# Optimization experiments

Measured on AMD Instinct MI355X. Metric: run time of the kernel, lower is better.

## Reference

```python
import jax, jax.numpy as jnp
import numpy as np

D_MODEL = 256
N_LAYER = 8
N_HEAD = 8
D_K = D_MODEL // N_HEAD  # 32
D_FF = 4 * D_MODEL
VOCAB = 5
NUM_BUCKETS = 64
MAX_DIST = 256
L = 768
B = 1
EPS = 1e-5


def _ln(x, s, b):
    m = jnp.mean(x, axis=-1, keepdims=True)
    v = jnp.mean((x - m) ** 2, axis=-1, keepdims=True)
    return (x - m) * jax.lax.rsqrt(v + EPS) * s + b


def _rp_bucket(rel_pos):
    # faithful to RelativePositionBias._relative_position_bucket
    nb = NUM_BUCKETS // 2  # 32
    ret = (rel_pos < 0).astype(jnp.int32) * nb
    arp = jnp.abs(rel_pos)
    max_exact = nb // 2  # 16
    is_small = arp < max_exact
    safe = jnp.maximum(arp, 1).astype(jnp.float32)
    log_ratio = float(np.log(MAX_DIST / max_exact))
    vil = max_exact + (jnp.log(safe / max_exact) / log_ratio * (nb - max_exact)).astype(jnp.int32)
    vil = jnp.minimum(vil, nb - 1)
    return ret + jnp.where(is_small, arp.astype(jnp.int32), vil)


def setup_inputs() -> dict:
    key = jax.random.key(0)
    ks = iter(jax.random.split(key, 40))
    s = 0.02
    d = {}
    d['seq'] = jax.random.randint(next(ks), (B, L), 0, VOCAB, dtype=jnp.int32)
    d['tok_emb'] = jax.random.normal(next(ks), (VOCAB, D_MODEL), jnp.float32) * s
    d['rp_emb'] = jax.random.normal(next(ks), (NUM_BUCKETS, N_HEAD), jnp.float32) * s
    # stacked per-layer params [N_LAYER, ...]
    d['wq'] = jax.random.normal(next(ks), (N_LAYER, D_MODEL, D_MODEL), jnp.float32) * s
    d['wk'] = jax.random.normal(next(ks), (N_LAYER, D_MODEL, D_MODEL), jnp.float32) * s
    d['wv'] = jax.random.normal(next(ks), (N_LAYER, D_MODEL, D_MODEL), jnp.float32) * s
    d['wo'] = jax.random.normal(next(ks), (N_LAYER, D_MODEL, D_MODEL), jnp.float32) * s
    d['ln1_s'] = jnp.ones((N_LAYER, D_MODEL), jnp.float32)
    d['ln1_b'] = jnp.zeros((N_LAYER, D_MODEL), jnp.float32)
    d['ln2_s'] = jnp.ones((N_LAYER, D_MODEL), jnp.float32)
    d['ln2_b'] = jnp.zeros((N_LAYER, D_MODEL), jnp.float32)
    d['ffn_w1'] = jax.random.normal(next(ks), (N_LAYER, D_MODEL, D_FF), jnp.float32) * s
    d['ffn_b1'] = jnp.zeros((N_LAYER, D_FF), jnp.float32)
    d['ffn_w2'] = jax.random.normal(next(ks), (N_LAYER, D_FF, D_MODEL), jnp.float32) * s
    d['ffn_b2'] = jnp.zeros((N_LAYER, D_MODEL), jnp.float32)
    d['lnf_s'] = jnp.ones((D_MODEL,), jnp.float32)
    d['lnf_b'] = jnp.zeros((D_MODEL,), jnp.float32)
    d['pair_q_w'] = jax.random.normal(next(ks), (D_MODEL, D_MODEL), jnp.float32) * s
    d['pair_q_b'] = jnp.zeros((D_MODEL,), jnp.float32)
    d['pair_k_w'] = jax.random.normal(next(ks), (D_MODEL, D_MODEL), jnp.float32) * s
    d['pair_k_b'] = jnp.zeros((D_MODEL,), jnp.float32)
    d['pair_rp_emb'] = jax.random.normal(next(ks), (NUM_BUCKETS, D_MODEL), jnp.float32) * s
    d['cls_w1'] = jax.random.normal(next(ks), (D_MODEL, D_MODEL), jnp.float32) * s
    d['cls_b1'] = jnp.zeros((D_MODEL,), jnp.float32)
    d['cls_w2'] = jax.random.normal(next(ks), (D_MODEL, 2), jnp.float32) * s
    d['cls_b2'] = jnp.zeros((2,), jnp.float32)
    return d


def reference(seq, tok_emb, rp_emb, wq, wk, wv, wo, ln1_s, ln1_b, ln2_s, ln2_b,
              ffn_w1, ffn_b1, ffn_w2, ffn_b2, lnf_s, lnf_b,
              pair_q_w, pair_q_b, pair_k_w, pair_k_b, pair_rp_emb,
              cls_w1, cls_b1, cls_w2, cls_b2):
    scale = D_K ** 0.5
    x = tok_emb[seq]  # [B, L, D]
    pos = jnp.arange(L)
    rel = pos[:, None] - pos[None, :]  # [L, L]
    bucket = _rp_bucket(rel)  # [L, L] int32
    bias = jnp.transpose(rp_emb[bucket], (2, 0, 1))[None]  # [1, H, L, L]

    def step(x, p):
        Wq, Wk, Wv, Wo, s1, b1, s2, b2, fw1, fb1, fw2, fb2 = p
        h = _ln(x, s1, b1)
        q = (h @ Wq).reshape(B, L, N_HEAD, D_K).transpose(0, 2, 1, 3)
        k = (h @ Wk).reshape(B, L, N_HEAD, D_K).transpose(0, 2, 1, 3)
        v = (h @ Wv).reshape(B, L, N_HEAD, D_K).transpose(0, 2, 1, 3)
        attn = jnp.einsum('bhid,bhjd->bhij', q / scale, k) + bias
        attn = jax.nn.softmax(attn, axis=-1)
        o = jnp.einsum('bhij,bhjd->bhid', attn, v)
        o = o.transpose(0, 2, 1, 3).reshape(B, L, D_MODEL) @ Wo
        x = x + o
        h2 = _ln(x, s2, b2)
        f = jax.nn.gelu(h2 @ fw1 + fb1, approximate=False) @ fw2 + fb2
        return x + f, None

    x, _ = jax.lax.scan(step, x, (wq, wk, wv, wo, ln1_s, ln1_b, ln2_s, ln2_b,
                                  ffn_w1, ffn_b1, ffn_w2, ffn_b2))
    x = _ln(x, lnf_s, lnf_b)
    q = x @ pair_q_w + pair_q_b  # [B, L, D]
    k = x @ pair_k_w + pair_k_b
    px = jnp.einsum('bic,bjc->bijc', q, k)  # [B, L, L, D]
    px = px + pair_rp_emb[bucket][None]  # add [L, L, D] pair rel-pos embedding
    px = jax.nn.relu(px @ cls_w1 + cls_b1) @ cls_w2 + cls_b2  # [B, L, L, 2]
    return px
```

## Files before the change

kernel.cpp:

```cpp
#include <hip/hip_runtime.h>
#include <hip/hip_bf16.h>
#include <stdint.h>

#define LSEQ 768
#define DM   256
#define NH   8
#define DK   32
#define DFF  1024
#define NLAYER 8
#define NDD  1535

typedef __attribute__((ext_vector_type(8))) short     bf16x8;
typedef __attribute__((ext_vector_type(8))) _Float16  f16x8;
typedef __attribute__((ext_vector_type(4))) float     f32x4;

__device__ __forceinline__ unsigned short f2bf(float f) {
  unsigned u = __float_as_uint(f);
  u += 0x7fffu + ((u >> 16) & 1u);
  return (unsigned short)(u >> 16);
}
__device__ __forceinline__ unsigned short f2h(float f) {
  union { _Float16 h; unsigned short s; } c;
  c.h = (_Float16)f;
  return c.s;
// ... 58 lines not shown
  int mg = m0 + arow;
  int mgc = mg < M ? mg : M - 1;
  const float* Ar = (GR == 1) ? (gsrc + (size_t)seqIdx[mgc] * K)
                              : (gsrc + (size_t)bucket_of(mgc) * K);
  float mean = 0.f, rstd = 0.f;
  if (LN) {
    int lq = t & 3;
    float s = 0.f, s2 = 0.f;
    const float* p = Ar + lq * 64;
    #pragma unroll
    for (int c = 0; c < 64; c += 4) {
      float4 v = *(const float4*)(p + c);
      s  += v.x + v.y + v.z + v.w;
      s2 += v.x * v.x + v.y * v.y + v.z * v.z + v.w * v.w;
    }
    red[arow][lq] = s; red[arow][lq + 4] = s2;
    __syncthreads();
    if (lq == 0) {
      float sm = red[arow][0] + red[arow][1] + red[arow][2] + red[arow][3];
      float sq = red[arow][4] + red[arow][5] + red[arow][6] + red[arow][7];
      float m = sm * (1.f / 256.f);
      float v = sq * (1.f / 256.f) - m * m;
      stat[arow][0] = m;
      stat[arow][1] = rsqrtf(v + 1e-5f);
    }
    __syncthreads();
    mean = stat[arow][0]; rstd = stat[arow][1];
  }

  int bkr = t >> 3, bn8 = (t & 7) * 8;
  int ty = t >> 4, tx = t & 15;
  float acc[4][4] = {};
  int nk = K >> 5;

  for (int kt = 0; kt < nk; ++kt) {
    int k0 = kt << 5;
    float4 a0 = *(const float4*)(Ar + k0 + akq);
    float4 a1 = *(const float4*)(Ar + k0 + akq + 4);
    if (LN) {
      float4 ls0 = *(const float4*)(lns + k0 + akq), ls1 = *(const float4*)(lns + k0 + akq + 4);
      float4 lb0 = *(const float4*)(lnb + k0 + akq), lb1 = *(const float4*)(lnb + k0 + akq + 4);
      a0.x=(a0.x-mean)*rstd*ls0.x+lb0.x; a0.y=(a0.y-mean)*rstd*ls0.y+lb0.y;
      a0.z=(a0.z-mean)*rstd*ls0.z+lb0.z; a0.w=(a0.w-mean)*rstd*ls0.w+lb0.w;
      a1.x=(a1.x-mean)*rstd*ls1.x+lb1.x; a1.y=(a1.y-mean)*rstd*ls1.y+lb1.y;
      a1.z=(a1.z-mean)*rstd*ls1.z+lb1.z; a1.w=(a1.w-mean)*rstd*ls1.w+lb1.w;
    }
    int cur = kt & 1;
    As[cur][akq+0][arow]=a0.x; As[cur][akq+1][arow]=a0.y; As[cur][akq+2][arow]=a0.z; As[cur][akq+3][arow]=a0.w;
    As[cur][akq+4][arow]=a1.x; As[cur][akq+5][arow]=a1.y; As[cur][akq+6][arow]=a1.z; As[cur][akq+7][arow]=a1.w;
    *(float4*)&Bs[cur][bkr][bn8] = *(const float4*)(B + (size_t)(k0 + bkr) * N + n0 + bn8);
    *(float4*)&Bs[cur][bkr][bn8+4] = *(const float4*)(B + (size_t)(k0 + bkr) * N + n0 + bn8 + 4);
    __syncthreads();
    #pragma unroll 8
    for (int kk = 0; kk < 32; ++kk) {
      float4 a = *(float4*)&As[cur][kk][ty * 4];
      float4 b = *(float4*)&Bs[cur][kk][tx * 4];
      acc[0][0]=fmaf(a.x,b.x,acc[0][0]); acc[0][1]=fmaf(a.x,b.y,acc[0][1]);
      acc[0][2]=fmaf(a.x,b.z,acc[0][2]); acc[0][3]=fmaf(a.x,b.w,acc[0][3]);
      acc[1][0]=fmaf(a.y,b.x,acc[1][0]); acc[1][1]=fmaf(a.y,b.y,acc[1][1]);
      acc[1][2]=fmaf(a.y,b.z,acc[1][2]); acc[1][3]=fmaf(a.y,b.w,acc[1][3]);
      acc[2][0]=fmaf(a.z,b.x,acc[2][0]); acc[2][1]=fmaf(a.z,b.y,acc[2][1]);
      acc[2][2]=fmaf(a.z,b.z,acc[2][2]); acc[2][3]=fmaf(a.z,b.w,acc[2][3]);
      acc[3][0]=fmaf(a.w,b.x,acc[3][0]); acc[3][1]=fmaf(a.w,b.y,acc[3][1]);
      acc[3][2]=fmaf(a.w,b.z,acc[3][2]); acc[3][3]=fmaf(a.w,b.w,acc[3][3]);
    }
    __syncthreads();
  }

  #pragma unroll
  for (int u = 0; u < 4; ++u) {
    int m = m0 + ty * 4 + u;
    if (m < M) {
      int n = n0 + tx * 4;
      float4 val = make_float4(acc[u][0], acc[u][1], acc[u][2], acc[u][3]);
      if (bias) {
        float4 bv = *(const float4*)(bias + n);
        val.x += bv.x; val.y += bv.y; val.z += bv.z; val.w += bv.w;
      }
      *(float4*)(C + (size_t)m * N + n) = val;
    }
  }
}

__global__ __launch_bounds__(256, 2) void k_prep(
    const int* __restrict__ seq, const float* __restrict__ tok_emb,
    const float* __restrict__ rp_emb,
    const float* __restrict__ wq, const float* __restrict__ wk,
    const float* __restrict__ wv, const float* __restrict__ wo,
    const float* __restrict__ ffn_w1, const float* __restrict__ ffn_w2,
    const float* __restrict__ ln1s0, const float* __restrict__ ln1b0,
    const float* __restrict__ pair_rp, const float* __restrict__ cls_w1,
    const float* __restrict__ cls_b1,
    const float* __restrict__ pair_q_w, const float* __restrict__ pair_k_w,
    float* x0, float* q0, float* k0, float* v0, float* RB,
    unsigned short* W1p, float* abias,
    unsigned short* Wop, unsigned short* W1pk, unsigned short* W2pk,
    unsigned short* Wqkvp, unsigned short* Wpairp) {
  __shared__ __align__(16) char sm[37376];
  int b = blockIdx.x, t = threadIdx.x;
  if (b < 96) {
    int m0 = (b % 24) * 64, n0 = (b / 24) * 64;
    gemm_tile<0,2>(pair_rp, nullptr, cls_w1, cls_b1, RB,
                   nullptr, nullptr, NDD, 256, 256, m0, n0, sm);
  } else if (b < 240) {
    int u = b - 96;
    int n0g = (u % 12) * 64, m0 = (u / 12) * 64;
    int bi = n0g >> 8, n0 = n0g & 255;
    const float* B = bi == 0 ? wq : (bi == 1 ? wk : wv);
    float* C = bi == 0 ? q0 : (bi == 1 ? k0 : v0);
    gemm_tile<1,1>(tok_emb, seq, B, nullptr, C,
                   ln1s0, ln1b0, LSEQ, 256, 256, m0, n0, sm);
  } else if (b < 432) {
    int row = (b - 240) * 4 + (t >> 6), c = (t & 63) * 4;
    *(float4*)(x0 + (size_t)row * DM + c) =
        *(const float4*)(tok_emb + (size_t)seq[row] * DM + c);
  } else if (b < 438) {
    int dd = (b - 432) * 256 + t;
    if (dd < NDD) {
      int bk = bucket_of(dd);
      #pragma unroll
      for (int h = 0; h < NH; ++h) abias[dd * 8 + h] = rp_emb[bk * 8 + h];
    }
  } else if (b < 502) {
    int base = (b - 438) * 1024 + t * 4;
    #pragma unroll
    for (int uu = 0; uu < 4; ++uu) {
      int id = base + uu;
      int e = id & 7, lane = (id >> 3) & 63, g = (id >> 9) & 15, kc = id >> 13;
      int kg = kc * 32 + (lane >> 4) * 8 + e;
      int n  = g * 16 + (lane & 15);
      W1p[id] = f2bf(cls_w1[(size_t)kg * 256 + n]);
    }
  } else {
    int u = (b - 502) * 2048 + t * 8;
    if (u < 524288) {
      int layer = u >> 16, id = u & 65535;
      pack8h(Wop + ((size_t)layer << 16), id, wo + ((size_t)layer << 16), 256, 16);
    } else if (u < 2621440) {
      int v2 = u - 524288; int layer = v2 >> 18, id = v2 & 262143;
      pack8h(W1pk + ((size_t)layer << 18), id, ffn_w1 + ((size_t)layer << 18), 1024, 64);
    } else if (u < 4718592) {
      int v2 = u - 2621440; int layer = v2 >> 18, id = v2 & 262143;
      pack8h(W2pk + ((size_t)layer << 18), id, ffn_w2 + ((size_t)layer << 18), 256, 16);
    } else if (u < 6291456) {
      int v2 = u - 4718592; int layer = v2 / 196608, id = v2 - layer * 196608;
      pack8h_cat(Wqkvp + (size_t)layer * 196608, id,
                 wq + ((size_t)layer << 16), wk + ((size_t)layer << 16),
                 wv + ((size_t)layer << 16), 48);
    } else {
      int id = u - 6291456;
      pack8h_cat(Wpairp, id, pair_q_w, pair_k_w, pair_k_w, 32);
    }
  }
}

#define ATTN_SMEM 72960

__global__ __launch_bounds__(256, 2) void k_attn2(
    const float* __restrict__ q, const float* __restrict__ k,
    const float* __restrict__ v, const float* __restrict__ abias,
    float* __restrict__ o) {
  extern __shared__ char sm[];
  float* S  = (float*)sm;
  float* KV = (float*)(sm + 49664);
  float* QS = (float*)(sm + 66560);
  float* BS = (float*)(sm + 68672);
  float (*red)[16] = (float (*)[16])(sm + 71808);
  float* mrow = (float*)(sm + 72832);
  float* linv = (float*)(sm + 72896);

  int i0 = blockIdx.x * 16, h = blockIdx.y, hc = h * DK;
  int t = threadIdx.x;

  for (int u = t; u < 783; u += 256)
    BS[u] = abias[(size_t)(i0 + u) * 8 + h];
  {
    int r = t >> 4, c = t & 15;
    const float inv = 0.17677669529663687f;
    QS[r * 33 + c]      = q[(size_t)(i0 + r) * DM + hc + c] * inv;
    QS[r * 33 + c + 16] = q[(size_t)(i0 + r) * DM + hc + c + 16] * inv;
  }

  int kx = t & 31, ry = t >> 5;
  int key = t >> 1, half = t & 1;

  for (int cc = 0; cc < 6; ++cc) {
    const float* kp = k + (size_t)(cc * 128 + key) * DM + hc + half * 16;
    float4 L0 = *(const float4*)(kp);
    float4 L1 = *(const float4*)(kp + 4);
    float4 L2 = *(const float4*)(kp + 8);
    float4 L3 = *(const float4*)(kp + 12);
    __syncthreads();
    int cb = half * 16;
    KV[(cb+ 0)*132+key]=L0.x; KV[(cb+ 1)*132+key]=L0.y; KV[(cb+ 2)*132+key]=L0.z; KV[(cb+ 3)*132+key]=L0.w;
    KV[(cb+ 4)*132+key]=L1.x; KV[(cb+ 5)*132+key]=L1.y; KV[(cb+ 6)*132+key]=L1.z; KV[(cb+ 7)*132+key]=L1.w;
    KV[(cb+ 8)*132+key]=L2.x; KV[(cb+ 9)*132+key]=L2.y; KV[(cb+10)*132+key]=L2.z; KV[(cb+11)*132+key]=L2.w;
    KV[(cb+12)*132+key]=L3.x; KV[(cb+13)*132+key]=L3.y; KV[(cb+14)*132+key]=L3.z; KV[(cb+15)*132+key]=L3.w;
    __syncthreads();

    float s0x=0,s0y=0,s0z=0,s0w=0, s1x=0,s1y=0,s1z=0,s1w=0;
    #pragma unroll
    for (int kk = 0; kk < 32; ++kk) {
      float q0 = QS[(ry*2    )*33 + kk];
      float q1 = QS[(ry*2 + 1)*33 + kk];
      float4 kv4 = *(const float4*)&KV[kk*132 + kx*4];
      s0x = fmaf(q0, kv4.x, s0x); s0y = fmaf(q0, kv4.y, s0y);
      s0z = fmaf(q0, kv4.z, s0z); s0w = fmaf(q0, kv4.w, s0w);
      s1x = fmaf(q1, kv4.x, s1x); s1y = fmaf(q1, kv4.y, s1y);
      s1z = fmaf(q1, kv4.z, s1z); s1w = fmaf(q1, kv4.w, s1w);
    }
    int jb = cc * 128 + kx * 4;
    int r0 = ry * 2, r1 = r0 + 1;
    S[r0*776 + jb+0] = s0x + BS[r0 + 767 - (jb+0)];
    S[r0*776 + jb+1] = s0y + BS[r0 + 767 - (jb+1)];
    S[r0*776 + jb+2] = s0z + BS[r0 + 767 - (jb+2)];
    S[r0*776 + jb+3] = s0w + BS[r0 + 767 - (jb+3)];
    S[r1*776 + jb+0] = s1x + BS[r1 + 767 - (jb+0)];
    S[r1*776 + jb+1] = s1y + BS[r1 + 767 - (jb+1)];
    S[r1*776 + jb+2] = s1z + BS[r1 + 767 - (jb+2)];
    S[r1*776 + jb+3] = s1w + BS[r1 + 767 - (jb+3)];
  }
  __syncthreads();

  {
    int ti = t >> 4, tj = t & 15;
    float mx = -1e30f;
    for (int jc = 0; jc < 48; ++jc)
      mx = fmaxf(mx, S[ti*776 + jc*16 + tj]);
    red[ti][tj] = mx;
    __syncthreads();
    if (tj == 0) {
      float m2 = red[ti][0];
      #pragma unroll
      for (int u = 1; u < 16; ++u) m2 = fmaxf(m2, red[ti][u]);
      mrow[ti] = m2;
    }
    __syncthreads();
    float m2 = mrow[ti];
    float sum = 0.f;
    for (int jc = 0; jc < 48; ++jc) {
      int j = jc*16 + tj;
      float e = __expf(S[ti*776 + j] - m2);
      S[ti*776 + j] = e;
      sum += e;
    }
    red[ti][tj] = sum;
    __syncthreads();
    if (tj == 0) {
      float s2 = 0.f;
      #pragma unroll
      for (int u = 0; u < 16; ++u) s2 += red[ti][u];
      linv[ti] = 1.f / s2;
    }
  }

  int cp = t & 15, jg = t >> 4;
  int c0 = cp * 2, c1 = c0 + 1;
  float oc0[16] = {}, oc1[16] = {};
  for (int cc = 0; cc < 6; ++cc) {
    const float* vp = v + (size_t)(cc * 128 + key) * DM + hc + half * 16;
    float4 L0 = *(const float4*)(vp);
    float4 L1 = *(const float4*)(vp + 4);
    float4 L2 = *(const float4*)(vp + 8);
    float4 L3 = *(const float4*)(vp + 12);
    __syncthreads();
    int cb = half * 16;
    KV[(cb+ 0)*132+key]=L0.x; KV[(cb+ 1)*132+key]=L0.y; KV[(cb+ 2)*132+key]=L0.z; KV[(cb+ 3)*132+key]=L0.w;
    KV[(cb+ 4)*132+key]=L1.x; KV[(cb+ 5)*132+key]=L1.y; KV[(cb+ 6)*132+key]=L1.z; KV[(cb+ 7)*132+key]=L1.w;
    KV[(cb+ 8)*132+key]=L2.x; KV[(cb+ 9)*132+key]=L2.y; KV[(cb+10)*132+key]=L2.z; KV[(cb+11)*132+key]=L2.w;
    KV[(cb+12)*132+key]=L3.x; KV[(cb+13)*132+key]=L3.y; KV[(cb+14)*132+key]=L3.z; KV[(cb+15)*132+key]=L3.w;
    __syncthreads();

    #pragma unroll
    for (int jj2 = 0; jj2 < 2; ++jj2) {
      int jb = jg * 8 + jj2 * 4;
      float4 vA = *(const float4*)&KV[c0*132 + jb];
      float4 vB = *(const float4*)&KV[c1*132 + jb];
      #pragma unroll
      for (int r = 0; r < 16; ++r) {
        float4 sv = *(const float4*)&S[r*776 + cc*128 + jb];
        oc0[r] += sv.x*vA.x + sv.y*vA.y + sv.z*vA.z + sv.w*vA.w;
        oc1[r] += sv.x*vB.x + sv.y*vB.y + sv.z*vB.z + sv.w*vB.w;
      }
    }
  }

  #pragma unroll
  for (int h2 = 0; h2 < 2; ++h2) {
    __syncthreads();
    #pragma unroll
    for (int r = 0; r < 8; ++r) {
      KV[(jg*8 + r)*32 + c0] = oc0[h2*8 + r];
      KV[(jg*8 + r)*32 + c1] = oc1[h2*8 + r];
    }
    __syncthreads();
    int r = t >> 5, c = t & 31;
    float s = 0.f;
    #pragma unroll
    for (int jgg = 0; jgg < 16; ++jgg) s += KV[(jgg*8 + r)*32 + c];
    o[(size_t)(i0 + h2*8 + r) * DM + hc + c] = s * linv[h2*8 + r];
  }
}

struct TC {
  const float* o; const float* xin;
  const unsigned short* wop;
  const float* ln2s; const float* ln2b;
  const unsigned short* w1p; const float* fb1;
  const unsigned short* w2p; const float* fb2;
  const unsigned short* wnp;
  const float* lns; const float* lnb;
  const float* nb0; const float* nb1;
  float *qo, *ko, *vo, *xo;
};

__device__ __forceinline__ void ln8(float (*Xf)[260], _Float16 (*Ab)[264],
                                    const float* s, const float* b, int t) {
  int r = t >> 6, j = t & 63;
  int c0 = j * 4;
  float4 x = *(const float4*)&Xf[r][c0];
  float s1 = x.x + x.y + x.z + x.w;
  float s2 = x.x*x.x + x.y*x.y + x.z*x.z + x.w*x.w;
  #pragma unroll
  for (int m = 1; m < 64; m <<= 1) {
    s1 += __shfl_xor(s1, m);
    s2 += __shfl_xor(s2, m);
  }
  float mean = s1 * (1.f / 256.f);
  float var  = s2 * (1.f / 256.f) - mean * mean;
  float rs = rsqrtf(var + 1e-5f);
  union { _Float16 h[4]; uint2 u; } cv;
  cv.h[0] = (_Float16)((x.x - mean) * rs * s[c0+0] + b[c0+0]);
  cv.h[1] = (_Float16)((x.y - mean) * rs * s[c0+1] + b[c0+1]);
  cv.h[2] = (_Float16)((x.z - mean) * rs * s[c0+2] + b[c0+2]);
  cv.h[3] = (_Float16)((x.w - mean) * rs * s[c0+3] + b[c0+3]);
  *(uint2*)&Ab[r][c0] = cv.u;
}

template <int LAST>
__global__ __launch_bounds__(512) void k_tail3(TC a) {
  __shared__ float    Xf[8][260];
  __shared__ _Float16 Ab[16][264];
  __shared__ _Float16 Fb[16][1032];

  int t = threadIdx.x;
  int i0 = blockIdx.x * 8;
  int w = t >> 6, l = t & 63;
  int lr = l & 15, lq = l >> 4;

  {
    int row = t >> 6, col = (t & 63) * 4;
    float4 v0 = *(const float4*)(a.o + (size_t)(i0 + row) * DM + col);
    union { _Float16 h[4]; uint2 u; } cv;
    cv.h[0] = (_Float16)v0.x; cv.h[1] = (_Float16)v0.y;
    cv.h[2] = (_Float16)v0.z; cv.h[3] = (_Float16)v0.w;
    *(uint2*)&Ab[row][col] = cv.u;
    *(float4*)&Xf[row][col] = *(const float4*)(a.xin + (size_t)(i0 + row) * DM + col);
    for (int z = t; z < 1056; z += 512) ((unsigned*)&Ab[8][0])[z] = 0;
  }
  __syncthreads();

  f16x8 af[8];
  #pragma unroll
  for (int kc = 0; kc < 8; ++kc)
    af[kc] = *(const f16x8*)&Ab[lr][kc * 32 + lq * 8];

  {
    const unsigned short* wp = a.wop + (size_t)l * 8;
    int g0 = w * 2, g1 = g0 + 1;
    f16x8 wb0[8], wb1[8];
    #pragma unroll
    for (int kc = 0; kc < 8; ++kc) {
      wb0[kc] = *(const f16x8*)(wp + ((kc * 16 + g0) << 9));
      wb1[kc] = *(const f16x8*)(wp + ((kc * 16 + g1) << 9));
    }
    f32x4 a0v = {0.f,0.f,0.f,0.f}, a1v = {0.f,0.f,0.f,0.f};
    #pragma unroll
    for (int kc = 0; kc < 8; ++kc) {
      a0v = __builtin_amdgcn_mfma_f32_16x16x32_f16(af[kc], wb0[kc], a0v, 0, 0, 0);
      a1v = __builtin_amdgcn_mfma_f32_16x16x32_f16(af[kc], wb1[kc], a1v, 0, 0, 0);
    }
    if (lq < 2) {
      #pragma unroll
      for (int r = 0; r < 4; ++r) {
        Xf[lq * 4 + r][g0 * 16 + lr] += a0v[r];
        Xf[lq * 4 + r][g1 * 16 + lr] += a1v[r];
      }
    }
  }
  __syncthreads();

  ln8(Xf, Ab, a.ln2s, a.ln2b, t);
  __syncthreads();

  #pragma unroll
  for (int kc = 0; kc < 8; ++kc)
    af[kc] = *(const f16x8*)&Ab[lr][kc * 32 + lq * 8];

  {
    const unsigned short* wp = a.w1p + (size_t)l * 8;
    f16x8 cur[8], nxt[8];
    #pragma unroll
    for (int kc = 0; kc < 8; ++kc)
      cur[kc] = *(const f16x8*)(wp + ((kc * 64 + w * 8) << 9));
    #pragma unroll
    for (int gi = 0; gi < 8; ++gi) {
      int g = w * 8 + gi;
      if (gi < 7) {
        #pragma unroll
        for (int kc = 0; kc < 8; ++kc)
          nxt[kc] = *(const f16x8*)(wp + ((kc * 64 + g + 1) << 9));
      }
      f32x4 ac = {0.f,0.f,0.f,0.f};
      #pragma unroll
      for (int kc = 0; kc < 8; ++kc)
        ac = __builtin_amdgcn_mfma_f32_16x16x32_f16(af[kc], cur[kc], ac, 0, 0, 0);
      int n = g * 16 + lr;
      float bb1 = a.fb1[n];
      #pragma unroll
      for (int r = 0; r < 4; ++r) {
        float v = ac[r] + bb1;
        v = 0.5f * v * (1.f + erff(v * 0.70710678118654752f));
        Fb[lq * 4 + r][n] = (_Float16)v;
      }
      if (gi < 7) {
        #pragma unroll
        for (int kc = 0; kc < 8; ++kc) cur[kc] = nxt[kc];
      }
    }
  }
  __syncthreads();

  {
    const unsigned short* wp = a.w2p + (size_t)l * 8;
    int g0 = w * 2, g1 = g0 + 1;
    f32x4 ac0 = {0.f,0.f,0.f,0.f}, ac1 = {0.f,0.f,0.f,0.f};
    f16x8 c0[8], c1[8], n0[8], n1[8];
    #pragma unroll
    for (int k8 = 0; k8 < 8; ++k8) {
      c0[k8] = *(const f16x8*)(wp + ((k8 * 16 + g0) << 9));
      c1[k8] = *(const f16x8*)(wp + ((k8 * 16 + g1) << 9));
    }
    #pragma unroll
    for (int bb = 0; bb < 4; ++bb) {
      if (bb < 3) {
        #pragma unroll
        for (int k8 = 0; k8 < 8; ++k8) {
          int kc = (bb + 1) * 8 + k8;
          n0[k8] = *(const f16x8*)(wp + ((kc * 16 + g0) << 9));
          n1[k8] = *(const f16x8*)(wp + ((kc * 16 + g1) << 9));
        }
      }
      #pragma unroll
      for (int k8 = 0; k8 < 8; ++k8) {
        int kc = bb * 8 + k8;
        f16x8 fa = *(const f16x8*)&Fb[lr][kc * 32 + lq * 8];
        ac0 = __builtin_amdgcn_mfma_f32_16x16x32_f16(fa, c0[k8], ac0, 0, 0, 0);
        ac1 = __builtin_amdgcn_mfma_f32_16x16x32_f16(fa, c1[k8], ac1, 0, 0, 0);
      }
      if (bb < 3) {
        #pragma unroll
        for (int k8 = 0; k8 < 8; ++k8) { c0[k8] = n0[k8]; c1[k8] = n1[k8]; }
      }
    }
    if (lq < 2) {
      int na = g0 * 16 + lr, nb = g1 * 16 + lr;
      float ba = a.fb2[na], bbv = a.fb2[nb];
      #pragma unroll
      for (int r = 0; r < 4; ++r) {
        int rr = lq * 4 + r;
        float xa = Xf[rr][na] + ac0[r] + ba;
        float xb = Xf[rr][nb] + ac1[r] + bbv;
        Xf[rr][na] = xa; Xf[rr][nb] = xb;
        a.xo[(size_t)(i0 + rr) * DM + na] = xa;
        a.xo[(size_t)(i0 + rr) * DM + nb] = xb;
      }
    }
  }
  __syncthreads();

  ln8(Xf, Ab, a.lns, a.lnb, t);
  __syncthreads();

  #pragma unroll
  for (int kc = 0; kc < 8; ++kc)
    af[kc] = *(const f16x8*)&Ab[lr][kc * 32 + lq * 8];

  if (!LAST) {
    const unsigned short* wp = a.wnp + (size_t)l * 8;
    f16x8 cur[8], nxt[8];
    #pragma unroll
    for (int kc = 0; kc < 8; ++kc)
      cur[kc] = *(const f16x8*)(wp + ((kc * 48 + w * 6) << 9));
    #pragma unroll
    for (int gi = 0; gi < 6; ++gi) {
      int g = w * 6 + gi;
      if (gi < 5) {
        #pragma unroll
        for (int kc = 0; kc < 8; ++kc)
          nxt[kc] = *(const f16x8*)(wp + ((kc * 48 + g + 1) << 9));
      }
      f32x4 ac = {0.f,0.f,0.f,0.f};
      #pragma unroll
      for (int kc = 0; kc < 8; ++kc)
        ac = __builtin_amdgcn_mfma_f32_16x16x32_f16(af[kc], cur[kc], ac, 0, 0, 0);
      if (lq < 2) {
        int n = g * 16 + lr;
        float* dst = n < 256 ? a.qo : (n < 512 ? a.ko : a.vo);
        int nn = n & 255;
        #pragma unroll
        for (int r = 0; r < 4; ++r)
          dst[(size_t)(i0 + lq * 4 + r) * DM + nn] = ac[r];
      }
      if (gi < 5) {
        #pragma unroll
        for (int kc = 0; kc < 8; ++kc) cur[kc] = nxt[kc];
      }
    }
  } else {
    const unsigned short* wp = a.wnp + (size_t)l * 8;
    f16x8 cur[8], nxt[8];
    #pragma unroll
    for (int kc = 0; kc < 8; ++kc)
      cur[kc] = *(const f16x8*)(wp + ((kc * 32 + w * 4) << 9));
    #pragma unroll
    for (int gi = 0; gi < 4; ++gi) {
      int g = w * 4 + gi;
      if (gi < 3) {
        #pragma unroll
        for (int kc = 0; kc < 8; ++kc)
          nxt[kc] = *(const f16x8*)(wp + ((kc * 32 + g + 1) << 9));
      }
      f32x4 ac = {0.f,0.f,0.f,0.f};
      #pragma unroll
      for (int kc = 0; kc < 8; ++kc)
        ac = __builtin_amdgcn_mfma_f32_16x16x32_f16(af[kc], cur[kc], ac, 0, 0, 0);
      if (lq < 2) {
        int n = g * 16 + lr;
        float* dst = n < 256 ? a.qo : a.ko;
        const float* bias = n < 256 ? a.nb0 : a.nb1;
        int nn = n & 255;
        float bv = bias[nn];
        #pragma unroll
        for (int r = 0; r < 4; ++r)
          dst[(size_t)(i0 + lq * 4 + r) * DM + nn] = ac[r] + bv;
      }
      if (gi < 3) {
        #pragma unroll
        for (int kc = 0; kc < 8; ++kc) cur[kc] = nxt[kc];
      }
    }
  }
}

#define PAIR_SMEM 74864

__global__ __launch_bounds__(256, 2) void k_pair(
    const float* __restrict__ pq, const float* __restrict__ pk,
    const unsigned short* __restrict__ W1p, const float* __restrict__ RB,
    const float* __restrict__ w2, const float* __restrict__ b2,
    float* __restrict__ out) {
  extern __shared__ char smem[];
  float* qs   = (float*)smem;
  float* ks   = (float*)(smem + 4160);
  float* RB_s = (float*)(smem + 37440);
  float* racc = (float*)(smem + 73840);

  int t = threadIdx.x;
  int j0 = blockIdx.x * 32;
  int i0 = blockIdx.y * 4;
  int w = t >> 6, l = t & 63;
  int q4 = l >> 4, l15 = l & 15;
  int mwv = w & 1, nwv = w >> 1;

  {
    int row = t >> 6, c4 = (t & 63) * 4;
    *(float4*)(qs + row * 260 + c4) = *(const float4*)(pq + (size_t)(i0 + row) * DM + c4);
    #pragma unroll
    for (int r8 = 0; r8 < 8; ++r8) {
      int idx = t + r8 * 256;
      int kr = idx >> 6, kc4 = (idx & 63) * 4;
      *(float4*)(ks + kr * 260 + kc4) = *(const float4*)(pk + (size_t)(j0 + kr) * DM + kc4);
    }
    int ddmin = i0 - j0 + 736;
    for (int idx = t; idx < 35 * 64; idx += 256) {
      int lc = idx >> 6, c4b = (idx & 63) * 4;
      *(float4*)(RB_s + lc * 260 + c4b) =
          *(const float4*)(RB + (size_t)(ddmin + lc) * 256 + c4b);
    }
    racc[t] = 0.f;
  }
  __syncthreads();

  const unsigned short* Bp = W1p + (size_t)(nwv * 8) * 512 + (size_t)l * 8;
  const float* q0p = qs + (mwv * 2) * 260;
  const float* q1p = qs + (mwv * 2 + 1) * 260;
  const float* k0p = ks + l15 * 260;
  const float* k1p = ks + (16 + l15) * 260;

  f32x4 acc[4][8];
  #pragma unroll
  for (int aa = 0; aa < 4; ++aa)
    #pragma unroll
    for (int bb = 0; bb < 8; ++bb) acc[aa][bb] = (f32x4){0.f, 0.f, 0.f, 0.f};

  bf16x8 bcur[8];
  #pragma unroll
  for (int nt = 0; nt < 8; ++nt) bcur[nt] = *(const bf16x8*)(Bp + nt * 512);

  for (int kc = 0; kc < 8; ++kc) {
    bf16x8 bnxt[8];
    if (kc < 7) {
      const unsigned short* bbn = Bp + (size_t)(kc + 1) * 8192;
      #pragma unroll
      for (int nt = 0; nt < 8; ++nt) bnxt[nt] = *(const bf16x8*)(bbn + nt * 512);
    }
    int c = kc * 32 + q4 * 8;
    float4 qa0 = *(const float4*)(q0p + c), qa1 = *(const float4*)(q0p + c + 4);
    float4 qb0 = *(const float4*)(q1p + c), qb1 = *(const float4*)(q1p + c + 4);
    float4 ka0 = *(const float4*)(k0p + c), ka1 = *(const float4*)(k0p + c + 4);
    float4 kb0 = *(const float4*)(k1p + c), kb1 = *(const float4*)(k1p + c + 4);

    union { bf16x8 v; unsigned u[4]; } af[4];
    af[0].u[0] = pk2(qa0.x*ka0.x, qa0.y*ka0.y); af[0].u[1] = pk2(qa0.z*ka0.z, qa0.w*ka0.w);
    af[0].u[2] = pk2(qa1.x*ka1.x, qa1.y*ka1.y); af[0].u[3] = pk2(qa1.z*ka1.z, qa1.w*ka1.w);
    af[1].u[0] = pk2(qa0.x*kb0.x, qa0.y*kb0.y); af[1].u[1] = pk2(qa0.z*kb0.z, qa0.w*kb0.w);
    af[1].u[2] = pk2(qa1.x*kb1.x, qa1.y*kb1.y); af[1].u[3] = pk2(qa1.z*kb1.z, qa1.w*kb1.w);
    af[2].u[0] = pk2(qb0.x*ka0.x, qb0.y*ka0.y); af[2].u[1] = pk2(qb0.z*ka0.z, qb0.w*ka0.w);
    af[2].u[2] = pk2(qb1.x*ka1.x, qb1.y*ka1.y); af[2].u[3] = pk2(qb1.z*ka1.z, qb1.w*ka1.w);
    af[3].u[0] = pk2(qb0.x*kb0.x, qb0.y*kb0.y); af[3].u[1] = pk2(qb0.z*kb0.z, qb0.w*kb0.w);
    af[3].u[2] = pk2(qb1.x*kb1.x, qb1.y*kb1.y); af[3].u[3] = pk2(qb1.z*kb1.z, qb1.w*kb1.w);

    #pragma unroll
    for (int mt = 0; mt < 4; ++mt)
      #pragma unroll
      for (int nt = 0; nt < 8; ++nt)
        acc[mt][nt] = __builtin_amdgcn_mfma_f32_16x16x32_bf16(af[mt].v, bcur[nt], acc[mt][nt], 0, 0, 0);
    if (kc < 7) {
      #pragma unroll
      for (int nt = 0; nt < 8; ++nt) bcur[nt] = bnxt[nt];
    }
  }

  float w20[8], w21[8];
  #pragma unroll
  for (int nt = 0; nt < 8; ++nt) {
    int n = nwv * 128 + nt * 16 + l15;
    w20[nt] = w2[n * 2];
    w21[nt] = w2[n * 2 + 1];
  }
  #pragma unroll
  for (int mt = 0; mt < 4; ++mt) {
    #pragma unroll
    for (int reg = 0; reg < 4; ++reg) {
      int r = mwv * 64 + mt * 16 + q4 * 4 + reg;
      int lc = (r >> 5) - (r & 31) + 31;
      float o0 = 0.f, o1 = 0.f;
      #pragma unroll
      for (int nt = 0; nt < 8; ++nt) {
        int n = nwv * 128 + nt * 16 + l15;
        float T = acc[mt][nt][reg] + RB_s[lc * 260 + n];
        T = fmaxf(T, 0.f);
        o0 = fmaf(T, w20[nt], o0);
        o1 = fmaf(T, w21[nt], o1);
      }
      #pragma unroll
      for (int s = 1; s < 16; s <<= 1) {
        o0 += __shfl_xor(o0, s);
        o1 += __shfl_xor(o1, s);
      }
      if (l15 == 0) {
        atomicAdd(&racc[r * 2 + 0], o0);
        atomicAdd(&racc[r * 2 + 1], o1);
      }
    }
  }
  __syncthreads();
  {
    int r = t >> 1, oo = t & 1;
    out[((size_t)(i0 + (r >> 5)) * LSEQ + (j0 + (r & 31))) * 2 + oo] = racc[t] + b2[oo];
  }
}

extern "C" void kernel_launch(void* const* d_in, const int* in_sizes, int n_in,
                              void* d_out, int out_size, void* d_ws, size_t ws_size,
                              hipStream_t stream) {
  const int*   seq      = (const int*)  d_in[0];
  const float* tok_emb  = (const float*)d_in[1];
  const float* rp_emb   = (const float*)d_in[2];
  const float* wq       = (const float*)d_in[3];
  const float* wk       = (const float*)d_in[4];
  const float* wv       = (const float*)d_in[5];
  const float* wo       = (const float*)d_in[6];
  const float* ln1_s    = (const float*)d_in[7];
  const float* ln1_b    = (const float*)d_in[8];
  const float* ln2_s    = (const float*)d_in[9];
  const float* ln2_b    = (const float*)d_in[10];
  const float* ffn_w1   = (const float*)d_in[11];
  const float* ffn_b1   = (const float*)d_in[12];
  const float* ffn_w2   = (const float*)d_in[13];
  const float* ffn_b2   = (const float*)d_in[14];
  const float* lnf_s    = (const float*)d_in[15];
  const float* lnf_b    = (const float*)d_in[16];
  const float* pair_q_w = (const float*)d_in[17];
  const float* pair_q_b = (const float*)d_in[18];
  const float* pair_k_w = (const float*)d_in[19];
  const float* pair_k_b = (const float*)d_in[20];
  const float* pair_rp  = (const float*)d_in[21];
  const float* cls_w1   = (const float*)d_in[22];
  const float* cls_b1   = (const float*)d_in[23];
  const float* cls_w2   = (const float*)d_in[24];
  const float* cls_b2   = (const float*)d_in[25];
  float* out = (float*)d_out;

  char* ws = (char*)d_ws;
  float* xb0 = (float*)(ws + 0);
  float* xb1 = (float*)(ws + 786432);
  float* qb[2] = { (float*)(ws + 1572864), (float*)(ws + 3932160) };
  float* kb[2] = { (float*)(ws + 2359296), (float*)(ws + 4718592) };
  float* vb[2] = { (float*)(ws + 3145728), (float*)(ws + 5505024) };
  float* o   = (float*)(ws + 6291456);
  float* pq  = (float*)(ws + 7077888);
  float* pk  = (float*)(ws + 7864320);
  float* RB  = (float*)(ws + 8650752);
  unsigned short* W1p = (unsigned short*)(ws + 10223616);
  float* abias = (float*)(ws + 10354688);
  unsigned short* Wop    = (unsigned short*)(ws + 10403840);
  unsigned short* W1pk   = (unsigned short*)(ws + 11452416);
  unsigned short* W2pk   = (unsigned short*)(ws + 15646720);
  unsigned short* Wqkvp  = (unsigned short*)(ws + 19841024);
  unsigned short* Wpairp = (unsigned short*)(ws + 22986752);

  (void)in_sizes; (void)n_in; (void)out_size; (void)ws_size;

  hipFuncSetAttribute(reinterpret_cast<const void*>(k_pair),
                      hipFuncAttributeMaxDynamicSharedMemorySize, PAIR_SMEM);
  hipFuncSetAttribute(reinterpret_cast<const void*>(k_attn2),
                      hipFuncAttributeMaxDynamicSharedMemorySize, ATTN_SMEM);

  k_prep<<<3638, 256, 0, stream>>>(seq, tok_emb, rp_emb, wq, wk, wv, wo,
                                   ffn_w1, ffn_w2, ln1_s, ln1_b,
                                   pair_rp, cls_w1, cls_b1, pair_q_w, pair_k_w,
                                   xb0, qb[0], kb[0], vb[0], RB, W1p, abias,
                                   Wop, W1pk, W2pk, Wqkvp, Wpairp);

  for (int l = 0; l < NLAYER; ++l) {
    int pi = l & 1, po = pi ^ 1;
    float* xin  = (l & 1) ? xb1 : xb0;
    float* xout = (l & 1) ? xb0 : xb1;

    k_attn2<<<dim3(48, 8), 256, ATTN_SMEM, stream>>>(qb[pi], kb[pi], vb[pi], abias, o);

    TC a{};
    a.o = o; a.xin = xin; a.xo = xout;
    a.wop = Wop + ((size_t)l << 16);
    a.ln2s = ln2_s + l * DM; a.ln2b = ln2_b + l * DM;
    a.w1p = W1pk + ((size_t)l << 18); a.fb1 = ffn_b1 + (size_t)l * DFF;
    a.w2p = W2pk + ((size_t)l << 18); a.fb2 = ffn_b2 + (size_t)l * DM;
    if (l < NLAYER - 1) {
      a.wnp = Wqkvp + (size_t)(l + 1) * 196608;
      a.lns = ln1_s + (l + 1) * DM; a.lnb = ln1_b + (l + 1) * DM;
      a.qo = qb[po]; a.ko = kb[po]; a.vo = vb[po];
      k_tail3<0><<<96, 512, 0, stream>>>(a);
    } else {
      a.wnp = Wpairp;
      a.nb0 = pair_q_b; a.nb1 = pair_k_b;
      a.lns = lnf_s; a.lnb = lnf_b;
      a.qo = pq; a.ko = pk;
      k_tail3<1><<<96, 512, 0, stream>>>(a);
    }
  }

  k_pair<<<dim3(24, 192), 256, PAIR_SMEM, stream>>>(pq, pk, W1p, RB, cls_w2, cls_b2, out);
}
```

Measured before the change: 658.1 us.

## Split fused layer tail into three kernels with 16-row tiles and column-split grids

Replaces the single 96-block k_tail3 (8 real rows padded to 16 per MFMA tile) with three kernels (Wo+LN2+FFN1, FFN2+residual, LN+next QKV), each launched on a 48x4 grid of 256-thread blocks. Every tile now uses all 16 MFMA rows instead of half, and the output columns are split across blockIdx.y, giving 192 blocks per launch instead of 96. The cost is two extra launches per layer, a round trip of the FFN hidden activations through global memory in fp16, and redundant Wo/LN2 compute repeated in each of the four y-blocks. Register-level weight prefetching is also dropped.

```diff
diff --git a/kernel.cpp b/kernel.cpp
--- a/kernel.cpp
+++ b/kernel.cpp
@@ -384,61 +384,33 @@
   }
 }
 
-struct TC {
-  const float* o; const float* xin;
-  const unsigned short* wop;
-  const float* ln2s; const float* ln2b;
-  const unsigned short* w1p; const float* fb1;
-  const unsigned short* w2p; const float* fb2;
-  const unsigned short* wnp;
-  const float* lns; const float* lnb;
-  const float* nb0; const float* nb1;
-  float *qo, *ko, *vo, *xo;
-};
-
-__device__ __forceinline__ void ln8(float (*Xf)[260], _Float16 (*Ab)[264],
-                                    const float* s, const float* b, int t) {
-  int r = t >> 6, j = t & 63;
-  int c0 = j * 4;
-  float4 x = *(const float4*)&Xf[r][c0];
-  float s1 = x.x + x.y + x.z + x.w;
-  float s2 = x.x*x.x + x.y*x.y + x.z*x.z + x.w*x.w;
-  #pragma unroll
-  for (int m = 1; m < 64; m <<= 1) {
-    s1 += __shfl_xor(s1, m);
-    s2 += __shfl_xor(s2, m);
-  }
-  float mean = s1 * (1.f / 256.f);
-  float var  = s2 * (1.f / 256.f) - mean * mean;
-  float rs = rsqrtf(var + 1e-5f);
-  union { _Float16 h[4]; uint2 u; } cv;
-  cv.h[0] = (_Float16)((x.x - mean) * rs * s[c0+0] + b[c0+0]);
-  cv.h[1] = (_Float16)((x.y - mean) * rs * s[c0+1] + b[c0+1]);
-  cv.h[2] = (_Float16)((x.z - mean) * rs * s[c0+2] + b[c0+2]);
-  cv.h[3] = (_Float16)((x.w - mean) * rs * s[c0+3] + b[c0+3]);
-  *(uint2*)&Ab[r][c0] = cv.u;
-}
-
-template <int LAST>
-__global__ __launch_bounds__(512) void k_tail3(TC a) {
-  __shared__ float    Xf[8][260];
-  __shared__ _Float16 Ab[16][264];
-  __shared__ _Float16 Fb[16][1032];
-
+
+__global__ __launch_bounds__(256, 2) void k_t1(
+    const float* __restrict__ o, const float* __restrict__ xin,
+    const unsigned short* __restrict__ wop,
+    const float* __restrict__ ln2s, const float* __restrict__ ln2b,
+    const unsigned short* __restrict__ w1p, const float* __restrict__ fb1,
+    float* __restrict__ x1, unsigned short* __restrict__ Fg) {
+  __shared__ __align__(16) float    Xf[16][260];
+  __shared__ __align__(16) _Float16 Ab[16][264];
   int t = threadIdx.x;
-  int i0 = blockIdx.x * 8;
+  int i0 = blockIdx.x * 16;
+  int by = blockIdx.y;
   int w = t >> 6, l = t & 63;
   int lr = l & 15, lq = l >> 4;
 
   {
-    int row = t >> 6, col = (t & 63) * 4;
-    float4 v0 = *(const float4*)(a.o + (size_t)(i0 + row) * DM + col);
-    union { _Float16 h[4]; uint2 u; } cv;
-    cv.h[0] = (_Float16)v0.x; cv.h[1] = (_Float16)v0.y;
-    cv.h[2] = (_Float16)v0.z; cv.h[3] = (_Float16)v0.w;
-    *(uint2*)&Ab[row][col] = cv.u;
-    *(float4*)&Xf[row][col] = *(const float4*)(a.xin + (size_t)(i0 + row) * DM + col);
-    for (int z = t; z < 1056; z += 512) ((unsigned*)&Ab[8][0])[z] = 0;
+    int r = t >> 4, j = t & 15;
+    #pragma unroll
+    for (int q = 0; q < 4; ++q) {
+      int c = j * 4 + q * 64;
+      float4 v = *(const float4*)(o + (size_t)(i0 + r) * DM + c);
+      union { _Float16 h[4]; uint2 u; } cv;
+      cv.h[0] = (_Float16)v.x; cv.h[1] = (_Float16)v.y;
+      cv.h[2] = (_Float16)v.z; cv.h[3] = (_Float16)v.w;
+      *(uint2*)&Ab[r][c] = cv.u;
+      *(float4*)&Xf[r][c] = *(const float4*)(xin + (size_t)(i0 + r) * DM + c);
+    }
   }
   __syncthreads();
 
@@ -448,31 +420,61 @@
     af[kc] = *(const f16x8*)&Ab[lr][kc * 32 + lq * 8];
 
   {
-    const unsigned short* wp = a.wop + (size_t)l * 8;
-    int g0 = w * 2, g1 = g0 + 1;
-    f16x8 wb0[8], wb1[8];
-    #pragma unroll
-    for (int kc = 0; kc < 8; ++kc) {
-      wb0[kc] = *(const f16x8*)(wp + ((kc * 16 + g0) << 9));
-      wb1[kc] = *(const f16x8*)(wp + ((kc * 16 + g1) << 9));
-    }
-    f32x4 a0v = {0.f,0.f,0.f,0.f}, a1v = {0.f,0.f,0.f,0.f};
-    #pragma unroll
-    for (int kc = 0; kc < 8; ++kc) {
-      a0v = __builtin_amdgcn_mfma_f32_16x16x32_f16(af[kc], wb0[kc], a0v, 0, 0, 0);
-      a1v = __builtin_amdgcn_mfma_f32_16x16x32_f16(af[kc], wb1[kc], a1v, 0, 0, 0);
-    }
-    if (lq < 2) {
-      #pragma unroll
-      for (int r = 0; r < 4; ++r) {
-        Xf[lq * 4 + r][g0 * 16 + lr] += a0v[r];
-        Xf[lq * 4 + r][g1 * 16 + lr] += a1v[r];
-      }
+    const unsigned short* wp = wop + (size_t)l * 8;
+    #pragma unroll
+    for (int gi = 0; gi < 4; ++gi) {
+      int g = w * 4 + gi;
+      f32x4 ac = {0.f, 0.f, 0.f, 0.f};
+      #pragma unroll
+      for (int kc = 0; kc < 8; ++kc) {
+        f16x8 bb = *(const f16x8*)(wp + ((kc * 16 + g) << 9));
+        ac = __builtin_amdgcn_mfma_f32_16x16x32_f16(af[kc], bb, ac, 0, 0, 0);
+      }
+      int n = g * 16 + lr;
+      #pragma unroll
+      for (int r = 0; r < 4; ++r)
+        Xf[lq * 4 + r][n] += ac[r];
     }
   }
   __syncthreads();
 
-  ln8(Xf, Ab, a.ln2s, a.ln2b, t);
+  if (by == 0) {
+    int r = t >> 4, j = t & 15;
+    #pragma unroll
+    for (int q = 0; q < 4; ++q) {
+      int c = j * 4 + q * 64;
+      *(float4*)(x1 + (size_t)(i0 + r) * DM + c) = *(const float4*)&Xf[r][c];
+    }
+  }
+
+  {
+    int r = t >> 4, j = t & 15;
+    int c0 = j * 16;
+    float xv[16]; float s1 = 0.f, s2 = 0.f;
+    #pragma unroll
+    for (int u = 0; u < 16; ++u) {
+      xv[u] = Xf[r][c0 + u];
+      s1 += xv[u]; s2 += xv[u] * xv[u];
+    }
+    #pragma unroll
+    for (int m = 1; m < 16; m <<= 1) {
+      s1 += __shfl_xor(s1, m);
+      s2 += __shfl_xor(s2, m);
+    }
+    float mean = s1 * (1.f / 256.f);
+    float var  = s2 * (1.f / 256.f) - mean * mean;
+    float rs = rsqrtf(var + 1e-5f);
+    #pragma unroll
+    for (int p = 0; p < 4; ++p) {
+      union { _Float16 h[4]; uint2 u; } cv;
+      #pragma unroll
+      for (int e = 0; e < 4; ++e) {
+        int c = c0 + p * 4 + e;
+        cv.h[e] = (_Float16)((xv[p * 4 + e] - mean) * rs * ln2s[c] + ln2b[c]);
+      }
+      *(uint2*)&Ab[r][c0 + p * 4] = cv.u;
+    }
+  }
   __syncthreads();
 
   #pragma unroll
@@ -480,157 +482,159 @@
     af[kc] = *(const f16x8*)&Ab[lr][kc * 32 + lq * 8];
 
   {
-    const unsigned short* wp = a.w1p + (size_t)l * 8;
-    f16x8 cur[8], nxt[8];
-    #pragma unroll
-    for (int kc = 0; kc < 8; ++kc)
-      cur[kc] = *(const f16x8*)(wp + ((kc * 64 + w * 8) << 9));
-    #pragma unroll
-    for (int gi = 0; gi < 8; ++gi) {
-      int g = w * 8 + gi;
-      if (gi < 7) {
-        #pragma unroll
-        for (int kc = 0; kc < 8; ++kc)
-          nxt[kc] = *(const f16x8*)(wp + ((kc * 64 + g + 1) << 9));
-      }
-      f32x4 ac = {0.f,0.f,0.f,0.f};
-      #pragma unroll
-      for (int kc = 0; kc < 8; ++kc)
-        ac = __builtin_amdgcn_mfma_f32_16x16x32_f16(af[kc], cur[kc], ac, 0, 0, 0);
+    const unsigned short* wp = w1p + (size_t)l * 8;
+    #pragma unroll
+    for (int gi = 0; gi < 4; ++gi) {
+      int g = by * 16 + w * 4 + gi;
+      f32x4 ac = {0.f, 0.f, 0.f, 0.f};
+      #pragma unroll
+      for (int kc = 0; kc < 8; ++kc) {
+        f16x8 bb = *(const f16x8*)(wp + ((kc * 64 + g) << 9));
+        ac = __builtin_amdgcn_mfma_f32_16x16x32_f16(af[kc], bb, ac, 0, 0, 0);
+      }
       int n = g * 16 + lr;
-      float bb1 = a.fb1[n];
+      float b1 = fb1[n];
       #pragma unroll
       for (int r = 0; r < 4; ++r) {
-        float v = ac[r] + bb1;
+        float v = ac[r] + b1;
         v = 0.5f * v * (1.f + erff(v * 0.70710678118654752f));
-        Fb[lq * 4 + r][n] = (_Float16)v;
-      }
-      if (gi < 7) {
-        #pragma unroll
-        for (int kc = 0; kc < 8; ++kc) cur[kc] = nxt[kc];
-      }
+        Fg[(size_t)(i0 + lq * 4 + r) * DFF + n] = f2h(v);
+      }
+    }
+  }
+}
+
+__global__ __launch_bounds__(256, 2) void k_t2(
+    const unsigned short* __restrict__ Fg, const float* __restrict__ x1,
+    const unsigned short* __restrict__ w2p, const float* __restrict__ fb2,
+    float* __restrict__ x2) {
+  __shared__ __align__(16) _Float16 Fs[16][1032];
+  int t = threadIdx.x;
+  int i0 = blockIdx.x * 16;
+  int by = blockIdx.y;
+  int w = t >> 6, l = t & 63;
+  int lr = l & 15, lq = l >> 4;
+
+  {
+    int r = t >> 4, j = t & 15;
+    #pragma unroll
+    for (int q = 0; q < 8; ++q) {
+      int c = j * 8 + q * 128;
+      *(uint4*)&Fs[r][c] = *(const uint4*)(Fg + (size_t)(i0 + r) * DFF + c);
     }
   }
   __syncthreads();
 
-  {
-    const unsigned short* wp = a.w2p + (size_t)l * 8;
-    int g0 = w * 2, g1 = g0 + 1;
-    f32x4 ac0 = {0.f,0.f,0.f,0.f}, ac1 = {0.f,0.f,0.f,0.f};
-    f16x8 c0[8], c1[8], n0[8], n1[8];
-    #pragma unroll
-    for (int k8 = 0; k8 < 8; ++k8) {
-      c0[k8] = *(const f16x8*)(wp + ((k8 * 16 + g0) << 9));
-      c1[k8] = *(const f16x8*)(wp + ((k8 * 16 + g1) << 9));
-    }
-    #pragma unroll
-    for (int bb = 0; bb < 4; ++bb) {
-      if (bb < 3) {
-        #pragma unroll
-        for (int k8 = 0; k8 < 8; ++k8) {
-          int kc = (bb + 1) * 8 + k8;
-          n0[k8] = *(const f16x8*)(wp + ((kc * 16 + g0) << 9));
-          n1[k8] = *(const f16x8*)(wp + ((kc * 16 + g1) << 9));
-        }
-      }
-      #pragma unroll
-      for (int k8 = 0; k8 < 8; ++k8) {
-        int kc = bb * 8 + k8;
-        f16x8 fa = *(const f16x8*)&Fb[lr][kc * 32 + lq * 8];
-        ac0 = __builtin_amdgcn_mfma_f32_16x16x32_f16(fa, c0[k8], ac0, 0, 0, 0);
-        ac1 = __builtin_amdgcn_mfma_f32_16x16x32_f16(fa, c1[k8], ac1, 0, 0, 0);
-      }
-      if (bb < 3) {
-        #pragma unroll
-        for (int k8 = 0; k8 < 8; ++k8) { c0[k8] = n0[k8]; c1[k8] = n1[k8]; }
-      }
-    }
-    if (lq < 2) {
-      int na = g0 * 16 + lr, nb = g1 * 16 + lr;
-      float ba = a.fb2[na], bbv = a.fb2[nb];
-      #pragma unroll
-      for (int r = 0; r < 4; ++r) {
-        int rr = lq * 4 + r;
-        float xa = Xf[rr][na] + ac0[r] + ba;
-        float xb = Xf[rr][nb] + ac1[r] + bbv;
-        Xf[rr][na] = xa; Xf[rr][nb] = xb;
-        a.xo[(size_t)(i0 + rr) * DM + na] = xa;
-        a.xo[(size_t)(i0 + rr) * DM + nb] = xb;
-      }
+  int g = by * 4 + w;
+  const unsigned short* wp = w2p + (size_t)l * 8;
+  f32x4 ac0 = {0.f, 0.f, 0.f, 0.f}, ac1 = {0.f, 0.f, 0.f, 0.f};
+  #pragma unroll
+  for (int kc = 0; kc < 32; kc += 2) {
+    f16x8 fa0 = *(const f16x8*)&Fs[lr][kc * 32 + lq * 8];
+    f16x8 bb0 = *(const f16x8*)(wp + ((kc * 16 + g) << 9));
+    ac0 = __builtin_amdgcn_mfma_f32_16x16x32_f16(fa0, bb0, ac0, 0, 0, 0);
+    f16x8 fa1 = *(const f16x8*)&Fs[lr][(kc + 1) * 32 + lq * 8];
+    f16x8 bb1 = *(const f16x8*)(wp + (((kc + 1) * 16 + g) << 9));
+    ac1 = __builtin_amdgcn_mfma_f32_16x16x32_f16(fa1, bb1, ac1, 0, 0, 0);
+  }
+  int n = g * 16 + lr;
+  float b2v = fb2[n];
+  #pragma unroll
+  for (int r = 0; r < 4; ++r) {
+    int row = i0 + lq * 4 + r;
+    x2[(size_t)row * DM + n] =
+        x1[(size_t)row * DM + n] + ac0[r] + ac1[r] + b2v;
+  }
+}
+
+template <int LAST>
+__global__ __launch_bounds__(256, 2) void k_t3(
+    const float* __restrict__ x2,
+    const float* __restrict__ lns, const float* __restrict__ lnb,
+    const unsigned short* __restrict__ wnp,
+    const float* __restrict__ nb0, const float* __restrict__ nb1,
+    float* __restrict__ qo, float* __restrict__ ko, float* __restrict__ vo) {
+  __shared__ __align__(16) _Float16 Ab[16][264];
+  int t = threadIdx.x;
+  int i0 = blockIdx.x * 16;
+  int by = blockIdx.y;
+  int w = t >> 6, l = t & 63;
+  int lr = l & 15, lq = l >> 4;
+
+  {
+    int r = t >> 4, j = t & 15;
+    int c0 = j * 16;
+    const float* xp = x2 + (size_t)(i0 + r) * DM + c0;
+    float xv[16]; float s1 = 0.f, s2 = 0.f;
+    #pragma unroll
+    for (int u = 0; u < 16; u += 4) {
+      float4 v = *(const float4*)(xp + u);
+      xv[u] = v.x; xv[u+1] = v.y; xv[u+2] = v.z; xv[u+3] = v.w;
+      s1 += v.x + v.y + v.z + v.w;
+      s2 += v.x*v.x + v.y*v.y + v.z*v.z + v.w*v.w;
+    }
+    #pragma unroll
+    for (int m = 1; m < 16; m <<= 1) {
+      s1 += __shfl_xor(s1, m);
+      s2 += __shfl_xor(s2, m);
+    }
+    float mean = s1 * (1.f / 256.f);
+    float var  = s2 * (1.f / 256.f) - mean * mean;
+    float rs = rsqrtf(var + 1e-5f);
+    #pragma unroll
+    for (int p = 0; p < 4; ++p) {
+      union { _Float16 h[4]; uint2 u; } cv;
+      #pragma unroll
+      for (int e = 0; e < 4; ++e) {
+        int c = c0 + p * 4 + e;
+        cv.h[e] = (_Float16)((xv[p * 4 + e] - mean) * rs * lns[c] + lnb[c]);
+      }
+      *(uint2*)&Ab[r][c0 + p * 4] = cv.u;
     }
   }
   __syncthreads();
 
-  ln8(Xf, Ab, a.lns, a.lnb, t);
-  __syncthreads();
-
+  f16x8 af[8];
   #pragma unroll
   for (int kc = 0; kc < 8; ++kc)
     af[kc] = *(const f16x8*)&Ab[lr][kc * 32 + lq * 8];
 
+  const unsigned short* wp = wnp + (size_t)l * 8;
   if (!LAST) {
-    const unsigned short* wp = a.wnp + (size_t)l * 8;
-    f16x8 cur[8], nxt[8];
-    #pragma unroll
-    for (int kc = 0; kc < 8; ++kc)
-      cur[kc] = *(const f16x8*)(wp + ((kc * 48 + w * 6) << 9));
-    #pragma unroll
-    for (int gi = 0; gi < 6; ++gi) {
-      int g = w * 6 + gi;
-      if (gi < 5) {
-        #pragma unroll
-        for (int kc = 0; kc < 8; ++kc)
-          nxt[kc] = *(const f16x8*)(wp + ((kc * 48 + g + 1) << 9));
-      }
-      f32x4 ac = {0.f,0.f,0.f,0.f};
-      #pragma unroll
-      for (int kc = 0; kc < 8; ++kc)
-        ac = __builtin_amdgcn_mfma_f32_16x16x32_f16(af[kc], cur[kc], ac, 0, 0, 0);
-      if (lq < 2) {
-        int n = g * 16 + lr;
-        float* dst = n < 256 ? a.qo : (n < 512 ? a.ko : a.vo);
-        int nn = n & 255;
-        #pragma unroll
-        for (int r = 0; r < 4; ++r)
-          dst[(size_t)(i0 + lq * 4 + r) * DM + nn] = ac[r];
-      }
-      if (gi < 5) {
-        #pragma unroll
-        for (int kc = 0; kc < 8; ++kc) cur[kc] = nxt[kc];
-      }
+    #pragma unroll
+    for (int gi = 0; gi < 3; ++gi) {
+      int g = by * 12 + w * 3 + gi;
+      f32x4 ac = {0.f, 0.f, 0.f, 0.f};
+      #pragma unroll
+      for (int kc = 0; kc < 8; ++kc) {
+        f16x8 bb = *(const f16x8*)(wp + ((kc * 48 + g) << 9));
+        ac = __builtin_amdgcn_mfma_f32_16x16x32_f16(af[kc], bb, ac, 0, 0, 0);
+      }
+      int n = g * 16 + lr;
+      float* dst = n < 256 ? qo : (n < 512 ? ko : vo);
+      int nn = n & 255;
+      #pragma unroll
+      for (int r = 0; r < 4; ++r)
+        dst[(size_t)(i0 + lq * 4 + r) * DM + nn] = ac[r];
     }
   } else {
-    const unsigned short* wp = a.wnp + (size_t)l * 8;
-    f16x8 cur[8], nxt[8];
-    #pragma unroll
-    for (int kc = 0; kc < 8; ++kc)
-      cur[kc] = *(const f16x8*)(wp + ((kc * 32 + w * 4) << 9));
-    #pragma unroll
-    for (int gi = 0; gi < 4; ++gi) {
-      int g = w * 4 + gi;
-      if (gi < 3) {
-        #pragma unroll
-        for (int kc = 0; kc < 8; ++kc)
-          nxt[kc] = *(const f16x8*)(wp + ((kc * 32 + g + 1) << 9));
-      }
-      f32x4 ac = {0.f,0.f,0.f,0.f};
-      #pragma unroll
-      for (int kc = 0; kc < 8; ++kc)
-        ac = __builtin_amdgcn_mfma_f32_16x16x32_f16(af[kc], cur[kc], ac, 0, 0, 0);
-      if (lq < 2) {
-        int n = g * 16 + lr;
-        float* dst = n < 256 ? a.qo : a.ko;
-        const float* bias = n < 256 ? a.nb0 : a.nb1;
-        int nn = n & 255;
-        float bv = bias[nn];
-        #pragma unroll
-        for (int r = 0; r < 4; ++r)
-          dst[(size_t)(i0 + lq * 4 + r) * DM + nn] = ac[r] + bv;
-      }
-      if (gi < 3) {
-        #pragma unroll
-        for (int kc = 0; kc < 8; ++kc) cur[kc] = nxt[kc];
-      }
+    #pragma unroll
+    for (int gi = 0; gi < 2; ++gi) {
+      int g = by * 8 + w * 2 + gi;
+      f32x4 ac = {0.f, 0.f, 0.f, 0.f};
+      #pragma unroll
+      for (int kc = 0; kc < 8; ++kc) {
+        f16x8 bb = *(const f16x8*)(wp + ((kc * 32 + g) << 9));
+        ac = __builtin_amdgcn_mfma_f32_16x16x32_f16(af[kc], bb, ac, 0, 0, 0);
+      }
+      int n = g * 16 + lr;
+      float* dst = n < 256 ? qo : ko;
+      const float* bias = n < 256 ? nb0 : nb1;
+      int nn = n & 255;
+      float bv = bias[nn];
+      #pragma unroll
+      for (int r = 0; r < 4; ++r)
+        dst[(size_t)(i0 + lq * 4 + r) * DM + nn] = ac[r] + bv;
     }
   }
 }
@@ -812,6 +816,8 @@
   unsigned short* W2pk   = (unsigned short*)(ws + 15646720);
   unsigned short* Wqkvp  = (unsigned short*)(ws + 19841024);
   unsigned short* Wpairp = (unsigned short*)(ws + 22986752);
+  unsigned short* Fg     = (unsigned short*)(ws + 23248896);
+  float* x1buf           = (float*)(ws + 24821760);
 
   (void)in_sizes; (void)n_in; (void)out_size; (void)ws_size;
 
@@ -833,23 +839,24 @@
 
     k_attn2<<<dim3(48, 8), 256, ATTN_SMEM, stream>>>(qb[pi], kb[pi], vb[pi], abias, o);
 
-    TC a{};
-    a.o = o; a.xin = xin; a.xo = xout;
-    a.wop = Wop + ((size_t)l << 16);
-    a.ln2s = ln2_s + l * DM; a.ln2b = ln2_b + l * DM;
-    a.w1p = W1pk + ((size_t)l << 18); a.fb1 = ffn_b1 + (size_t)l * DFF;
-    a.w2p = W2pk + ((size_t)l << 18); a.fb2 = ffn_b2 + (size_t)l * DM;
+    k_t1<<<dim3(48, 4), 256, 0, stream>>>(
+        o, xin, Wop + ((size_t)l << 16),
+        ln2_s + l * DM, ln2_b + l * DM,
+        W1pk + ((size_t)l << 18), ffn_b1 + (size_t)l * DFF,
+        x1buf, Fg);
+
+    k_t2<<<dim3(48, 4), 256, 0, stream>>>(
+        Fg, x1buf, W2pk + ((size_t)l << 18), ffn_b2 + (size_t)l * DM, xout);
+
     if (l < NLAYER - 1) {
-      a.wnp = Wqkvp + (size_t)(l + 1) * 196608;
-      a.lns = ln1_s + (l + 1) * DM; a.lnb = ln1_b + (l + 1) * DM;
-      a.qo = qb[po]; a.ko = kb[po]; a.vo = vb[po];
-      k_tail3<0><<<96, 512, 0, stream>>>(a);
+      k_t3<0><<<dim3(48, 4), 256, 0, stream>>>(
+          xout, ln1_s + (l + 1) * DM, ln1_b + (l + 1) * DM,
+          Wqkvp + (size_t)(l + 1) * 196608, nullptr, nullptr,
+          qb[po], kb[po], vb[po]);
     } else {
-      a.wnp = Wpairp;
-      a.nb0 = pair_q_b; a.nb1 = pair_k_b;
-      a.lns = lnf_s; a.lnb = lnf_b;
-      a.qo = pq; a.ko = pk;
-      k_tail3<1><<<96, 512, 0, stream>>>(a);
+      k_t3<1><<<dim3(48, 4), 256, 0, stream>>>(
+          xout, lnf_s, lnf_b, Wpairp, pair_q_b, pair_k_b,
+          pq, pk, nullptr);
     }
   }
 
```

Result: no change. 653.1 us (-0.8%).
